# Kernel optimization log

Measured on AMD Instinct MI355X. Metric: run time of the kernel, lower is better.

The kernel has to match this reference:

```python
import jax, jax.numpy as jnp
import numpy as np

BS, EMB, RES = 256, 768, 14
N_MASKS, HID, OUT, N_PROJ = 16, 4096, 256, 4
BN_EPS = 1e-5


def setup_inputs() -> dict:
    key = jax.random.key(0)
    ks = jax.random.split(key, 8)
    x = jax.random.normal(ks[0], (BS, EMB, RES, RES), jnp.float32)
    # binary ROI masks over the 14x14 = 196 patch grid
    masks = (jax.random.uniform(ks[1], (BS, N_MASKS, RES * RES)) < 0.3).astype(jnp.float32)
    projection_idx = jax.random.randint(ks[2], (N_MASKS,), 0, N_PROJ, jnp.int32)
    mask_ids = jax.random.randint(ks[3], (BS, N_MASKS), 0, 100, jnp.int32)
    # stacked params for the N_PROJ MLP projectors
    W1 = jax.random.normal(ks[4], (N_PROJ, EMB, HID), jnp.float32) * 0.02
    b1 = jnp.zeros((N_PROJ, HID), jnp.float32)
    gamma = jnp.ones((N_PROJ, HID), jnp.float32)
    beta = jnp.zeros((N_PROJ, HID), jnp.float32)
    W2 = jax.random.normal(ks[5], (N_PROJ, HID, OUT), jnp.float32) * 0.02
    b2 = jnp.zeros((N_PROJ, OUT), jnp.float32)
    return {"x": x, "masks": masks, "projection_idx": projection_idx,
            "mask_ids": mask_ids, "W1": W1, "b1": b1, "gamma": gamma,
            "beta": beta, "W2": W2, "b2": b2}


def reference(x, masks, projection_idx, mask_ids, W1, b1, gamma, beta, W2, b2):
    bs, emb, hx, hy = x.shape
    # [bs, emb, hx, hy] -> [bs, hw, emb]
    emb_local = jnp.transpose(x, (0, 2, 3, 1)).reshape(bs, hx * hy, emb)
    # mask-normalized pooling:  pooled[b,n,:] = mean of embeddings inside mask n
    area = masks.sum(axis=-1, keepdims=True)
    smpl = masks / jnp.maximum(area, 1.0)
    pooled = smpl @ emb_local                       # [bs, n_masks, emb]
    # dense dispatch: run EVERY projector over all pooled tokens (as original)
    h = jnp.einsum('bne,peh->pbnh', pooled, W1) + b1[:, None, None, :]
    # BatchNorm1d in training mode over flattened (bs*n_masks) batch, per projector
    mu = h.mean(axis=(1, 2), keepdims=True)
    var = jnp.mean(jnp.square(h - mu), axis=(1, 2), keepdims=True)  # biased var
    h = (h - mu) * jax.lax.rsqrt(var + BN_EPS) * gamma[:, None, None, :] + beta[:, None, None, :]
    h = jax.nn.relu(h)
    o = jnp.einsum('pbnh,pho->pbno', h, W2) + b2[:, None, None, :]   # [P, bs, n, out]
    # keep only projector projection_idx[n] for mask-slot n (disjoint selection)
    n_proj = W1.shape[0]
    sel = (projection_idx[None, :] == jnp.arange(n_proj)[:, None]).astype(o.dtype)  # [P, n]
    xs = (o * sel[:, None, :, None]).sum(axis=0)     # [bs, n_masks, out]
    return (xs, mask_ids)
```

## Files before the change

kernel.cpp:

```cpp
#include <hip/hip_runtime.h>
#include <hip/hip_bf16.h>

#define BS 256
#define EMB 768
#define HW 196
#define NMASK 16
#define HID 4096
#define OUT 256
#define NPROJ 4
#define MROWS 4096

typedef __attribute__((ext_vector_type(8))) short bf16x8;
typedef __attribute__((ext_vector_type(4))) float f32x4;
typedef __attribute__((ext_vector_type(8))) unsigned short u16x8;

__device__ inline float bf2f(unsigned short u) {
    unsigned int x = ((unsigned int)u) << 16;
    return __builtin_bit_cast(float, x);
}
__device__ inline short f2bfs(float f) {
    return __builtin_bit_cast(short, __float2bfloat16(f));
}

#define GL16(gptr, lptr)                                                     \
    __builtin_amdgcn_global_load_lds(                                        \
        (const __attribute__((address_space(1))) void*)(gptr),               \
        (__attribute__((address_space(3))) void*)(lptr), 16, 0, 0)

__global__ __launch_bounds__(256) void pool2(
    const float* __restrict__ x, const float* __restrict__ masks,
    __hip_bfloat16* __restrict__ pooledG, float* __restrict__ mpB)
{
    __shared__ __align__(16) float xs[192 * 196];
    __shared__ __align__(16) short afr[7 * 64 * 8];
    __shared__ float inv[NMASK];
    const int ec = blockIdx.x & 3, b = blockIdx.x >> 2;
    const int tid = threadIdx.x, lane = tid & 63, w = tid >> 6;
    const float* mb = masks + (size_t)b * NMASK * HW;

    {
        const char* gsrc = (const char*)(x + ((size_t)b * EMB + ec * 192 + w * 48) * HW);
        char* ldst = (char*)xs + w * 37632;
        #pragma unroll
        for (int i = 0; i < 36; ++i)
            GL16(gsrc + (size_t)i * 1024 + (size_t)lane * 16, ldst + i * 1024);
        if (lane < 48)
            GL16(gsrc + (size_t)36 * 1024 + (size_t)lane * 16, ldst + 36 * 1024);
    }

    for (int s = tid; s < 7 * 64; s += 256) {
        int m = s & 15, kb = ((s >> 4) & 3) * 8 + (s >> 6) * 32;
        short v[8];
        #pragma unroll
        for (int j = 0; j < 8; ++j) {
            int kk = kb + j;
            v[j] = (kk < HW) ? f2bfs(mb[m * HW + kk]) : (short)0;
        }
        #pragma unroll
        for (int j = 0; j < 8; ++j) afr[s * 8 + j] = v[j];
    }
    if (tid >= 192) {
        int l = tid - 192, m = l >> 2, q = l & 3;
        float a = 0.f;
        for (int hw = q; hw < HW; hw += 4) a += mb[m * HW + hw];
        a += __shfl_xor(a, 1);
        a += __shfl_xor(a, 2);
        if (q == 0) inv[m] = 1.0f / fmaxf(a, 1.0f);
    }
    __syncthreads();

    const int lc = lane & 15, l4 = lane >> 4;
    const int ebase = ec * 192 + w * 48;
    const float* xw = xs + (size_t)(w * 48) * 196;
    const bf16x8* afv = (const bf16x8*)afr;
    f32x4 acc[3] = {};

    for (int kc = 0; kc < 6; ++kc) {
        bf16x8 af = afv[kc * 64 + lane];
        float4 u[3][2];
        #pragma unroll
        for (int t = 0; t < 3; ++t) {
            const float* xr = xw + (size_t)(t * 16 + lc) * 196 + kc * 32 + l4 * 8;
            u[t][0] = *(const float4*)(xr);
            u[t][1] = *(const float4*)(xr + 4);
        }
        #pragma unroll
        for (int t = 0; t < 3; ++t) {
            bf16x8 bf;
            bf[0] = f2bfs(u[t][0].x); bf[1] = f2bfs(u[t][0].y);
            bf[2] = f2bfs(u[t][0].z); bf[3] = f2bfs(u[t][0].w);
            bf[4] = f2bfs(u[t][1].x); bf[5] = f2bfs(u[t][1].y);
            bf[6] = f2bfs(u[t][1].z); bf[7] = f2bfs(u[t][1].w);
            acc[t] = __builtin_amdgcn_mfma_f32_16x16x32_bf16(af, bf, acc[t], 0, 0, 0);
        }
    }
    {
        bf16x8 af = afv[6 * 64 + lane];
        #pragma unroll
        for (int t = 0; t < 3; ++t) {
            bf16x8 bf = {};
            if (l4 == 0) {
                float4 u0 = *(const float4*)(xw + (size_t)(t * 16 + lc) * 196 + 192);
                bf[0] = f2bfs(u0.x); bf[1] = f2bfs(u0.y);
                bf[2] = f2bfs(u0.z); bf[3] = f2bfs(u0.w);
            }
            acc[t] = __builtin_amdgcn_mfma_f32_16x16x32_bf16(af, bf, acc[t], 0, 0, 0);
        }
    }

    #pragma unroll
    for (int t = 0; t < 3; ++t) {
        int e = ebase + t * 16 + lc;
        float msum = 0.f;
        #pragma unroll
        for (int j = 0; j < 4; ++j) {
            int m = l4 * 4 + j;
            float v = acc[t][j] * inv[m];
            msum += v;
            pooledG[((size_t)m * 256 + b) * EMB + e] = __float2bfloat16(v);
        }
        msum += __shfl_xor(msum, 16);
        msum += __shfl_xor(msum, 32);
        if (l4 == 0) mpB[(size_t)b * EMB + e] = msum;
    }
}

__global__ __launch_bounds__(256) void prep(
    const float* __restrict__ W1, const float* __restrict__ W2,
    const __hip_bfloat16* __restrict__ pg,
    __hip_bfloat16* __restrict__ W1T, __hip_bfloat16* __restrict__ W2T,
    __hip_bfloat16* __restrict__ pgT)
{
    __shared__ __align__(16) char sm[64 * 65 * 4];
    const int bid = blockIdx.x, tid = threadIdx.x;
    if (bid < 4096) {
        const float* src; __hip_bfloat16* dst; int R, C, x, y, z;
        if (bid < 3072) { z = bid / 768; int r = bid % 768; x = r % 64; y = r / 64;
                          src = W1; dst = W1T; R = EMB; C = HID; }
        else            { int b2 = bid - 3072; z = b2 / 256; int r = b2 % 256;
                          x = r % 4; y = r / 4; src = W2; dst = W2T; R = HID; C = OUT; }
        float (*tile)[65] = (float(*)[65])sm;
        const float* s = src + (size_t)z * R * C;
        __hip_bfloat16* d = dst + (size_t)z * R * C;
        const int c0 = x * 64, r0 = y * 64;
        for (int i = tid; i < 4096; i += 256) {
            int r = i >> 6, c = i & 63;
            tile[r][c] = s[(size_t)(r0 + r) * C + c0 + c];
        }
        __syncthreads();
        for (int i = tid; i < 4096; i += 256) {
            int c = i >> 6, r = i & 63;
            d[(size_t)(c0 + c) * R + r0 + r] = __float2bfloat16(tile[r][c]);
        }
    } else {
        const int b3 = bid - 4096;
        const int x = b3 % 12, y = b3 / 12;
        __hip_bfloat16 (*tile)[65] = (__hip_bfloat16(*)[65])sm;
        const int c0 = x * 64, r0 = y * 64;
        for (int i = tid; i < 4096; i += 256) {
            int r = i >> 6, c = i & 63;
            tile[r][c] = pg[(size_t)(r0 + r) * EMB + c0 + c];
        }
        __syncthreads();
        for (int i = tid; i < 4096; i += 256) {
            int c = i >> 6, r = i & 63;
            pgT[(size_t)(c0 + c) * MROWS + r0 + r] = tile[r][c];
        }
    }
}

__global__ __launch_bounds__(256) void cgemm(
    const __hip_bfloat16* __restrict__ PT, float* __restrict__ Cpart)
{
    __shared__ __align__(16) __hip_bfloat16 As[128 * 32];
    __shared__ __align__(16) __hip_bfloat16 Bs[128 * 32];
    const int tid = threadIdx.x, lane = tid & 63, wid = tid >> 6;
    const int n0 = blockIdx.x * 128, m0 = blockIdx.y * 128, kbase = blockIdx.z * 512;
    float* Cp = Cpart + (size_t)blockIdx.z * EMB * EMB;
    const int wr = wid >> 1, wc = wid & 1;
    const int l4 = lane >> 4, lc = lane & 15;

    f32x4 acc[4][4] = {};
    for (int k0 = kbase; k0 < kbase + 512; k0 += 32) {
        __syncthreads();
        #pragma unroll
        for (int r = 0; r < 2; ++r) {
            int t = r * 256 + tid;
            int row = t >> 2, ko = (t & 3) * 8;
            GL16(PT + (size_t)(m0 + row) * MROWS + k0 + ko, &As[(r * 256 + wid * 64) * 8]);
        }
        #pragma unroll
        for (int r = 0; r < 2; ++r) {
            int t = r * 256 + tid;
            int row = t >> 2, ko = (t & 3) * 8;
            GL16(PT + (size_t)(n0 + row) * MROWS + k0 + ko, &Bs[(r * 256 + wid * 64) * 8]);
        }
        __syncthreads();
        const bf16x8* Av = (const bf16x8*)As;
        const bf16x8* Bv = (const bf16x8*)Bs;
        bf16x8 a[4], b[4];
        #pragma unroll
        for (int m = 0; m < 4; ++m) a[m] = Av[(wr * 64 + m * 16 + lc) * 4 + l4];
        #pragma unroll
        for (int n = 0; n < 4; ++n) b[n] = Bv[(wc * 64 + n * 16 + lc) * 4 + l4];
        #pragma unroll
        for (int m = 0; m < 4; ++m)
            #pragma unroll
            for (int n = 0; n < 4; ++n)
                acc[m][n] = __builtin_amdgcn_mfma_f32_16x16x32_bf16(a[m], b[n], acc[m][n], 0, 0, 0);
    }
    #pragma unroll
    for (int m = 0; m < 4; ++m)
        #pragma unroll
        for (int n = 0; n < 4; ++n)
            #pragma unroll
            for (int j = 0; j < 4; ++j) {
                int row = m0 + wr * 64 + m * 16 + l4 * 4 + j;
                int col = n0 + wc * 64 + n * 16 + lc;
                Cp[(size_t)row * EMB + col] = acc[m][n][j];
            }
}

__global__ __launch_bounds__(256) void cvt_c(
    const float* __restrict__ Cpart, const float* __restrict__ mpB,
    __hip_bfloat16* __restrict__ Cbf, float* __restrict__ mp)
{
    const int bid = blockIdx.x, tid = threadIdx.x;
    if (bid < 576) {
        int i = (bid * 256 + tid) * 4;
        float sx = 0.f, sy = 0.f, sz = 0.f, sw = 0.f;
        #pragma unroll
        for (int kz = 0; kz < 8; ++kz) {
            float4 v = *(const float4*)(Cpart + (size_t)kz * EMB * EMB + i);
            sx += v.x; sy += v.y; sz += v.z; sw += v.w;
        }
        const float s = 1.0f / 4096.0f;
        Cbf[i + 0] = __float2bfloat16(sx * s);
        Cbf[i + 1] = __float2bfloat16(sy * s);
        Cbf[i + 2] = __float2bfloat16(sz * s);
        Cbf[i + 3] = __float2bfloat16(sw * s);
    } else {
        int e = (bid - 576) * 256 + tid;
        float s = 0.f;
        for (int b = 0; b < 256; ++b) s += mpB[(size_t)b * EMB + e];
        mp[e] = s * (1.0f / 4096.0f);
    }
}

__global__ __launch_bounds__(256) void ugemm(
    const __hip_bfloat16* __restrict__ W1T, const __hip_bfloat16* __restrict__ Cbf,
    const float* __restrict__ mp,
    float* __restrict__ Eh2p, float* __restrict__ Mup)
{
    __shared__ __align__(16) __hip_bfloat16 As[128 * 32];
    __shared__ __align__(16) __hip_bfloat16 Bs[128 * 32];
    const int tid = threadIdx.x, lane = tid & 63, wid = tid >> 6;
    const int n0 = blockIdx.x * 128, m0 = blockIdx.y * 128, p = blockIdx.z;
    const __hip_bfloat16* Ap = W1T + (size_t)p * HID * EMB;
    const int wr = wid >> 1, wc = wid & 1;
    const int l4 = lane >> 4, lc = lane & 15;

    f32x4 acc[4][4] = {};
    for (int k0 = 0; k0 < EMB; k0 += 32) {
        __syncthreads();
        #pragma unroll
        for (int r = 0; r < 2; ++r) {
            int t = r * 256 + tid;
            int row = t >> 2, ko = (t & 3) * 8;
            GL16(Ap + (size_t)(m0 + row) * EMB + k0 + ko, &As[(r * 256 + wid * 64) * 8]);
        }
        #pragma unroll
        for (int r = 0; r < 2; ++r) {
            int t = r * 256 + tid;
            int row = t >> 2, ko = (t & 3) * 8;
            GL16(Cbf + (size_t)(n0 + row) * EMB + k0 + ko, &Bs[(r * 256 + wid * 64) * 8]);
        }
        __syncthreads();
        const bf16x8* Av = (const bf16x8*)As;
        const bf16x8* Bv = (const bf16x8*)Bs;
        bf16x8 a[4], b[4];
        #pragma unroll
        for (int m = 0; m < 4; ++m) a[m] = Av[(wr * 64 + m * 16 + lc) * 4 + l4];
        #pragma unroll
        for (int n = 0; n < 4; ++n) b[n] = Bv[(wc * 64 + n * 16 + lc) * 4 + l4];
        #pragma unroll
        for (int m = 0; m < 4; ++m)
            #pragma unroll
            for (int n = 0; n < 4; ++n)
                acc[m][n] = __builtin_amdgcn_mfma_f32_16x16x32_bf16(a[m], b[n], acc[m][n], 0, 0, 0);
    }

    float mpv[4];
    #pragma unroll
    for (int n = 0; n < 4; ++n) mpv[n] = mp[n0 + wc * 64 + n * 16 + lc];
    #pragma unroll
    for (int m = 0; m < 4; ++m) {
        #pragma unroll
        for (int j = 0; j < 4; ++j) {
            int row = m0 + wr * 64 + m * 16 + l4 * 4 + j;
            const __hip_bfloat16* wrow = Ap + (size_t)row * EMB;
            float e2 = 0.f, mu = 0.f;
            #pragma unroll
            for (int n = 0; n < 4; ++n) {
                int col = n0 + wc * 64 + n * 16 + lc;
                float wv = bf2f(__builtin_bit_cast(unsigned short, wrow[col]));
                e2 += acc[m][n][j] * wv;
                mu += mpv[n] * wv;
            }
            e2 += __shfl_xor(e2, 1); e2 += __shfl_xor(e2, 2);
            e2 += __shfl_xor(e2, 4); e2 += __shfl_xor(e2, 8);
            mu += __shfl_xor(mu, 1); mu += __shfl_xor(mu, 2);
            mu += __shfl_xor(mu, 4); mu += __shfl_xor(mu, 8);
            if (lc == 0) {
                size_t idx = (((size_t)blockIdx.x * 2 + wc) * NPROJ + p) * HID + row;
                Eh2p[idx] = e2;
                Mup [idx] = mu;
            }
        }
    }
}

__global__ __launch_bounds__(512, 2) void gemm1_sel(
    const __hip_bfloat16* __restrict__ A, const __hip_bfloat16* __restrict__ W1T,
    const int* __restrict__ proj,
    const float* __restrict__ Eh2p, const float* __restrict__ Mup,
    const float* __restrict__ gamma, const float* __restrict__ beta,
    __hip_bfloat16* __restrict__ hrelu)
{
    __shared__ __align__(16) short LS[3 * 16384];
    __shared__ float sS[256], sT[256];
    const int tid = threadIdx.x, lane = tid & 63, w = tid >> 6;
    const int wr = w >> 2, wc = w & 3;
    const int lc = lane & 15, l4 = lane >> 4;
    const int n0 = blockIdx.x * 256, m0 = blockIdx.y * 256;
    const int p = proj[blockIdx.y];
    const __hip_bfloat16* Ag = A;
    const __hip_bfloat16* Bg = W1T + (size_t)p * HID * EMB;
    const bf16x8* LSv = (const bf16x8*)LS;

    if (tid < 256) {
        int col = n0 + tid;
        float e2 = 0.f, mu = 0.f;
        #pragma unroll
        for (int s = 0; s < 12; ++s) {
            e2 += Eh2p[((size_t)s * NPROJ + p) * HID + col];
            mu += Mup [((size_t)s * NPROJ + p) * HID + col];
        }
        float var = e2 - mu * mu;
        float is  = rsqrtf(fmaxf(var, 0.0f) + 1e-5f);
        float sc  = gamma[p * HID + col] * is;
        sS[tid] = sc;
        sT[tid] = beta[p * HID + col] - mu * sc;
    }

    auto STAGE = [&](int t) {
        const int sb = (t % 3) * 32768;
        #pragma unroll
        for (int ab = 0; ab < 2; ++ab) {
            const __hip_bfloat16* g = ab ? Bg : Ag;
            const int rbase = ab ? n0 : m0;
            #pragma unroll
            for (int i = 0; i < 2; ++i) {
                int c = (w * 2 + i) * 64 + lane;
                int row = c >> 2, ps = c & 3;
                int ls = ps ^ (row & 3);
                const __hip_bfloat16* src =
                    g + (size_t)(rbase + row) * EMB + t * 32 + ls * 8;
                GL16(src, (char*)LS + sb + ab * 16384 + (w * 2 + i) * 1024);
            }
        }
    };

    f32x4 acc[8][4] = {};

    STAGE(0);
    STAGE(1);
    asm volatile("s_waitcnt vmcnt(4)" ::: "memory");
    __builtin_amdgcn_s_barrier();

    for (int t = 0; t < 24; ++t) {
        if (t + 2 < 24) STAGE(t + 2);
        const int vb = (t % 3) * 2048;

        bf16x8 bfr[4];
        #pragma unroll
        for (int nf = 0; nf < 4; ++nf) {
            int rb = wc * 64 + nf * 16 + lc;
            bfr[nf] = LSv[vb + 1024 + rb * 4 + (l4 ^ (rb & 3))];
        }
        #pragma unroll
        for (int q = 0; q < 4; ++q) {
            bf16x8 afr[2];
            #pragma unroll
            for (int m2 = 0; m2 < 2; ++m2) {
                int ra = wr * 128 + (q * 2 + m2) * 16 + lc;
                afr[m2] = LSv[vb + ra * 4 + (l4 ^ (ra & 3))];
            }
            __builtin_amdgcn_s_setprio(1);
            #pragma unroll
            for (int m2 = 0; m2 < 2; ++m2)
                #pragma unroll
                for (int nf = 0; nf < 4; ++nf)
                    acc[q * 2 + m2][nf] = __builtin_amdgcn_mfma_f32_16x16x32_bf16(
                        afr[m2], bfr[nf], acc[q * 2 + m2][nf], 0, 0, 0);
            __builtin_amdgcn_s_setprio(0);
        }

        if (t + 2 < 24) {
            asm volatile("s_waitcnt vmcnt(4)" ::: "memory");
            __builtin_amdgcn_s_barrier();
        } else if (t + 2 == 24) {
            asm volatile("s_waitcnt vmcnt(0)" ::: "memory");
            __builtin_amdgcn_s_barrier();
        }
    }

    #pragma unroll
    for (int nf = 0; nf < 4; ++nf) {
        int cl = wc * 64 + nf * 16 + lc;
        int col = n0 + cl;
        float s = sS[cl];
        float tt = sT[cl];
        #pragma unroll
        for (int mf = 0; mf < 8; ++mf)
            #pragma unroll
            for (int j = 0; j < 4; ++j) {
                int row = m0 + wr * 128 + mf * 16 + l4 * 4 + j;
                float v = fmaxf(acc[mf][nf][j] * s + tt, 0.0f);
                hrelu[(size_t)row * HID + col] = __float2bfloat16(v);
            }
    }
}

__global__ __launch_bounds__(256) void gemm2(
    const __hip_bfloat16* __restrict__ Hn, const __hip_bfloat16* __restrict__ W2T,
    const int* __restrict__ proj, float* __restrict__ Opart)
{
    __shared__ __align__(16) __hip_bfloat16 As[128 * 32];
    __shared__ __align__(16) __hip_bfloat16 Bs[128 * 32];
    const int tid = threadIdx.x, lane = tid & 63, wid = tid >> 6;
    const int nmask = blockIdx.x;
    const int bc    = blockIdx.y;
    const int ct    = blockIdx.z >> 2, kz = blockIdx.z & 3;
    const int p = proj[nmask];
    const __hip_bfloat16* Ap = Hn + (size_t)(nmask * 256 + bc * 128) * HID;
    const __hip_bfloat16* Bp = W2T + ((size_t)p * OUT + ct * 128) * HID;
    float* Op = Opart + (size_t)kz * MROWS * OUT;
    const int wr = wid >> 1, wc = wid & 1;
    const int l4 = lane >> 4, lc = lane & 15;

    f32x4 acc[4][4] = {};
    for (int k0 = kz * 1024; k0 < kz * 1024 + 1024; k0 += 32) {
        __syncthreads();
        #pragma unroll
        for (int r = 0; r < 2; ++r) {
            int t = r * 256 + tid;
            int row = t >> 2, ko = (t & 3) * 8;
            GL16(Ap + (size_t)row * HID + k0 + ko, &As[(r * 256 + wid * 64) * 8]);
        }
        #pragma unroll
        for (int r = 0; r < 2; ++r) {
            int t = r * 256 + tid;
            int row = t >> 2, ko = (t & 3) * 8;
            GL16(Bp + (size_t)row * HID + k0 + ko, &Bs[(r * 256 + wid * 64) * 8]);
        }
        __syncthreads();
        const bf16x8* Av = (const bf16x8*)As;
        const bf16x8* Bv = (const bf16x8*)Bs;
        bf16x8 a[4], b[4];
        #pragma unroll
        for (int m = 0; m < 4; ++m) a[m] = Av[(wr * 64 + m * 16 + lc) * 4 + l4];
        #pragma unroll
        for (int n = 0; n < 4; ++n) b[n] = Bv[(wc * 64 + n * 16 + lc) * 4 + l4];
        #pragma unroll
        for (int m = 0; m < 4; ++m)
            #pragma unroll
            for (int n = 0; n < 4; ++n)
                acc[m][n] = __builtin_amdgcn_mfma_f32_16x16x32_bf16(a[m], b[n], acc[m][n], 0, 0, 0);
    }

    #pragma unroll
    for (int m = 0; m < 4; ++m)
        #pragma unroll
        for (int n = 0; n < 4; ++n)
            #pragma unroll
            for (int j = 0; j < 4; ++j) {
                int bb = bc * 128 + wr * 64 + m * 16 + l4 * 4 + j;
                int oc = ct * 128 + wc * 64 + n * 16 + lc;
                Op[((size_t)bb * NMASK + nmask) * OUT + oc] = acc[m][n][j];
            }
}

__global__ __launch_bounds__(256) void reduce_out(
    const float* __restrict__ Opart, const float* __restrict__ b2,
    const int* __restrict__ proj, const int* __restrict__ mids,
    float* __restrict__ out)
{
    int i = (blockIdx.x * 256 + threadIdx.x) * 4;
    float sx = 0.f, sy = 0.f, sz = 0.f, sw = 0.f;
    #pragma unroll
    for (int kz = 0; kz < 4; ++kz) {
        float4 v = *(const float4*)(Opart + (size_t)kz * MROWS * OUT + i);
        sx += v.x; sy += v.y; sz += v.z; sw += v.w;
    }
    int nm = (i >> 8) & 15;
    int p  = proj[nm];
    float4 bv = *(const float4*)(b2 + p * OUT + (i & 255));
    float4 r;
    r.x = sx + bv.x; r.y = sy + bv.y; r.z = sz + bv.z; r.w = sw + bv.w;
    *(float4*)(out + i) = r;
    if (blockIdx.x < 16) {
        int t = blockIdx.x * 256 + threadIdx.x;
        out[(size_t)MROWS * OUT + t] = (float)mids[t];
    }
}

extern "C" void kernel_launch(void* const* d_in, const int* in_sizes, int n_in,
                              void* d_out, int out_size, void* d_ws, size_t ws_size,
                              hipStream_t stream)
{
    const float* x     = (const float*)d_in[0];
    const float* masks = (const float*)d_in[1];
    const int*   proj  = (const int*)d_in[2];
    const int*   mids  = (const int*)d_in[3];
    const float* W1    = (const float*)d_in[4];
    const float* gamma = (const float*)d_in[6];
    const float* beta  = (const float*)d_in[7];
    const float* W2    = (const float*)d_in[8];
    const float* b2    = (const float*)d_in[9];
    float* out = (float*)d_out;

    char* ws = (char*)d_ws;
    __hip_bfloat16* pooledG = (__hip_bfloat16*)(ws);
    __hip_bfloat16* W1T     = (__hip_bfloat16*)(ws + 6291456);
    __hip_bfloat16* W2T     = (__hip_bfloat16*)(ws + 31457280);
    float*          mp      = (float*)(ws + 39845888);
    float*          Eh2p    = (float*)(ws + 39848960);
    float*          Mup     = (float*)(ws + 40635392);
    float*          mpB     = (float*)(ws + 41421824);
    char* R = ws + 42208256;
    __hip_bfloat16* pooledT = (__hip_bfloat16*)(R);
    float*          Cpart   = (float*)(R + 6291456);
    __hip_bfloat16* Cbf     = (__hip_bfloat16*)(R + 25165824);
    __hip_bfloat16* hrelu   = (__hip_bfloat16*)(R);
    float*          Opart   = (float*)(R + 33554432);

    pool2<<<1024, 256, 0, stream>>>(x, masks, pooledG, mpB);
    prep<<<4864, 256, 0, stream>>>(W1, W2, pooledG, W1T, W2T, pooledT);
    cgemm<<<dim3(6, 6, 8), 256, 0, stream>>>(pooledT, Cpart);
    cvt_c<<<579, 256, 0, stream>>>(Cpart, mpB, Cbf, mp);
    ugemm<<<dim3(6, 32, 4), 256, 0, stream>>>(W1T, Cbf, mp, Eh2p, Mup);
    gemm1_sel<<<dim3(HID / 256, MROWS / 256), 512, 0, stream>>>(pooledG, W1T, proj, Eh2p, Mup, gamma, beta, hrelu);
    gemm2<<<dim3(NMASK, 2, 8), 256, 0, stream>>>(hrelu, W2T, proj, Opart);
    reduce_out<<<(MROWS * OUT) / 1024, 256, 0, stream>>>(Opart, b2, proj, mids, out);
}
```

Before: 221.1 us.

## Pipeline pooling kernel with per-wave triple-buffered LDS staging

Replaces the pooling kernel that loaded a whole 192-channel slab into LDS before computing. The new version uses one block per batch element, and each wave walks 12 chunks of 16 channels through a three-slot LDS ring. It issues global_load_lds for chunk c+2 and waits on vmcnt for chunk c, so global loads overlap the MFMA pooling work. The intent is to hide the load latency of reading x, at the cost of fewer blocks (256) and reliance on hand-counted vmcnt values.

After: 206.2 us. 6.7% less time.

```diff
diff --git a/kernel.cpp b/kernel.cpp
--- a/kernel.cpp
+++ b/kernel.cpp
@@ -27,26 +27,30 @@
         (const __attribute__((address_space(1))) void*)(gptr),               \
         (__attribute__((address_space(3))) void*)(lptr), 16, 0, 0)
 
-__global__ __launch_bounds__(256) void pool2(
+__global__ __launch_bounds__(256) void pool_pipe(
     const float* __restrict__ x, const float* __restrict__ masks,
     __hip_bfloat16* __restrict__ pooledG, float* __restrict__ mpB)
 {
-    __shared__ __align__(16) float xs[192 * 196];
+    __shared__ __align__(16) float xs[37632];
     __shared__ __align__(16) short afr[7 * 64 * 8];
     __shared__ float inv[NMASK];
-    const int ec = blockIdx.x & 3, b = blockIdx.x >> 2;
+    const int b = blockIdx.x;
     const int tid = threadIdx.x, lane = tid & 63, w = tid >> 6;
+    const int lc = lane & 15, l4 = lane >> 4;
     const float* mb = masks + (size_t)b * NMASK * HW;
 
-    {
-        const char* gsrc = (const char*)(x + ((size_t)b * EMB + ec * 192 + w * 48) * HW);
-        char* ldst = (char*)xs + w * 37632;
-        #pragma unroll
-        for (int i = 0; i < 36; ++i)
-            GL16(gsrc + (size_t)i * 1024 + (size_t)lane * 16, ldst + i * 1024);
-        if (lane < 48)
-            GL16(gsrc + (size_t)36 * 1024 + (size_t)lane * 16, ldst + 36 * 1024);
-    }
+    auto STAGE = [&](int s, int c) {
+        const char* gsrc = (const char*)(x + ((size_t)b * EMB + w * 192 + c * 16) * HW);
+        char* ldst = (char*)xs + w * 37632 + s * 12544;
+        #pragma unroll
+        for (int i = 0; i < 12; ++i)
+            GL16(gsrc + i * 1024 + (size_t)lane * 16, ldst + i * 1024);
+        if (lane < 16)
+            GL16(gsrc + 12288 + (size_t)lane * 16, ldst + 12288);
+    };
+
+    STAGE(0, 0);
+    STAGE(1, 1);
 
     for (int s = tid; s < 7 * 64; s += 256) {
         int m = s & 15, kb = ((s >> 4) & 3) * 8 + (s >> 6) * 32;
@@ -69,53 +73,46 @@
     }
     __syncthreads();
 
-    const int lc = lane & 15, l4 = lane >> 4;
-    const int ebase = ec * 192 + w * 48;
-    const float* xw = xs + (size_t)(w * 48) * 196;
     const bf16x8* afv = (const bf16x8*)afr;
-    f32x4 acc[3] = {};
-
-    for (int kc = 0; kc < 6; ++kc) {
-        bf16x8 af = afv[kc * 64 + lane];
-        float4 u[3][2];
-        #pragma unroll
-        for (int t = 0; t < 3; ++t) {
-            const float* xr = xw + (size_t)(t * 16 + lc) * 196 + kc * 32 + l4 * 8;
-            u[t][0] = *(const float4*)(xr);
-            u[t][1] = *(const float4*)(xr + 4);
-        }
-        #pragma unroll
-        for (int t = 0; t < 3; ++t) {
+
+    for (int c = 0; c < 12; ++c) {
+        if (c + 2 < 12) STAGE((c + 2) % 3, c + 2);
+        if (c < 10)       asm volatile("s_waitcnt vmcnt(26)" ::: "memory");
+        else if (c == 10) asm volatile("s_waitcnt vmcnt(13)" ::: "memory");
+        else              asm volatile("s_waitcnt vmcnt(0)" ::: "memory");
+
+        const float* xw = (const float*)((const char*)xs + w * 37632 + (c % 3) * 12544);
+        f32x4 acc = {};
+        #pragma unroll
+        for (int kc = 0; kc < 6; ++kc) {
+            bf16x8 af = afv[kc * 64 + lane];
+            const float* xr = xw + (size_t)lc * 196 + kc * 32 + l4 * 8;
+            float4 u0 = *(const float4*)(xr);
+            float4 u1 = *(const float4*)(xr + 4);
             bf16x8 bf;
-            bf[0] = f2bfs(u[t][0].x); bf[1] = f2bfs(u[t][0].y);
-            bf[2] = f2bfs(u[t][0].z); bf[3] = f2bfs(u[t][0].w);
-            bf[4] = f2bfs(u[t][1].x); bf[5] = f2bfs(u[t][1].y);
-            bf[6] = f2bfs(u[t][1].z); bf[7] = f2bfs(u[t][1].w);
-            acc[t] = __builtin_amdgcn_mfma_f32_16x16x32_bf16(af, bf, acc[t], 0, 0, 0);
-        }
-    }
-    {
-        bf16x8 af = afv[6 * 64 + lane];
-        #pragma unroll
-        for (int t = 0; t < 3; ++t) {
+            bf[0] = f2bfs(u0.x); bf[1] = f2bfs(u0.y);
+            bf[2] = f2bfs(u0.z); bf[3] = f2bfs(u0.w);
+            bf[4] = f2bfs(u1.x); bf[5] = f2bfs(u1.y);
+            bf[6] = f2bfs(u1.z); bf[7] = f2bfs(u1.w);
+            acc = __builtin_amdgcn_mfma_f32_16x16x32_bf16(af, bf, acc, 0, 0, 0);
+        }
+        {
+            bf16x8 af = afv[6 * 64 + lane];
             bf16x8 bf = {};
             if (l4 == 0) {
-                float4 u0 = *(const float4*)(xw + (size_t)(t * 16 + lc) * 196 + 192);
+                float4 u0 = *(const float4*)(xw + (size_t)lc * 196 + 192);
                 bf[0] = f2bfs(u0.x); bf[1] = f2bfs(u0.y);
                 bf[2] = f2bfs(u0.z); bf[3] = f2bfs(u0.w);
             }
-            acc[t] = __builtin_amdgcn_mfma_f32_16x16x32_bf16(af, bf, acc[t], 0, 0, 0);
-        }
-    }
-
-    #pragma unroll
-    for (int t = 0; t < 3; ++t) {
-        int e = ebase + t * 16 + lc;
+            acc = __builtin_amdgcn_mfma_f32_16x16x32_bf16(af, bf, acc, 0, 0, 0);
+        }
+
+        int e = w * 192 + c * 16 + lc;
         float msum = 0.f;
         #pragma unroll
         for (int j = 0; j < 4; ++j) {
             int m = l4 * 4 + j;
-            float v = acc[t][j] * inv[m];
+            float v = acc[j] * inv[m];
             msum += v;
             pooledG[((size_t)m * 256 + b) * EMB + e] = __float2bfloat16(v);
         }
@@ -545,7 +542,7 @@
     __hip_bfloat16* hrelu   = (__hip_bfloat16*)(R);
     float*          Opart   = (float*)(R + 33554432);
 
-    pool2<<<1024, 256, 0, stream>>>(x, masks, pooledG, mpB);
+    pool_pipe<<<256, 256, 0, stream>>>(x, masks, pooledG, mpB);
     prep<<<4864, 256, 0, stream>>>(W1, W2, pooledG, W1T, W2T, pooledT);
     cgemm<<<dim3(6, 6, 8), 256, 0, stream>>>(pooledT, Cpart);
     cvt_c<<<579, 256, 0, stream>>>(Cpart, mpB, Cbf, mp);
```
